# Kernel optimization log

Measured on AMD Instinct MI355X. Metric: run time of the kernel, lower is better.

The kernel has to match this reference:

```python
import jax, jax.numpy as jnp
import numpy as np


def _to_complex(t):
    # last dim 2 = (real, imag) -> complex64
    return jax.lax.complex(t[..., 0], t[..., 1])


def setup_inputs() -> dict:
    key = jax.random.key(0)
    k1, k2, k3, k4 = jax.random.split(key, 4)
    N, C_out, C_in, H, Wf = 2, 64, 3, 256, 129  # Wf = 256//2 + 1 (rfft width)
    X = jax.random.normal(k1, (N, 1, C_in, H, Wf, 2), dtype=jnp.float32)
    D = jax.random.normal(k2, (N, C_out, C_in, H, Wf, 2), dtype=jnp.float32)
    Y = jax.random.normal(k3, (N, C_out, 1, H, Wf, 2), dtype=jnp.float32)
    # alpha is a positive penalty weight; offset away from 0 to avoid blow-up in Z/alpha
    alpha = jax.random.uniform(k4, (N, 1, 1, 1), dtype=jnp.float32) + 0.5
    x_size = np.array([256, 256], dtype=np.int64)  # spatial size for irfft2
    return {"X": X, "D": D, "Y": Y, "alpha": alpha, "x_size": x_size}


def reference(X, D, Y, alpha, x_size):
    C_in = X.shape[2]
    Xc = _to_complex(X)  # (N,1,C_in,H,Wf)
    Dc = _to_complex(D)  # (N,C_out,C_in,H,Wf)
    Yc = _to_complex(Y)  # (N,C_out,1,H,Wf)
    # alpha.unsqueeze(-1).unsqueeze(-1)/C_in: in complex repr one extra axis suffices
    a = (alpha / C_in)[..., None]  # (N,1,1,1,1), real, broadcasts over (N,C_out,C_in,H,Wf)
    Dconj = jnp.conj(Dc)
    Z = Yc * Dc + a * Xc  # (N,C_out,C_in,H,Wf)
    factor1 = Z / a
    numerator = jnp.sum(Dconj * Z, axis=2, keepdims=True)  # (N,C_out,1,H,Wf)
    # csum adds a real scalar (alpha^2) to the real part only
    denominator = a * jnp.sum(Dconj * Dc, axis=2, keepdims=True) + a ** 2
    factor2 = Dc * (numerator / denominator)  # (N,C_out,C_in,H,Wf)
    Xhat = jnp.mean(factor1 - factor2, axis=1)  # (N,C_in,H,Wf)
    Hs, Ws = int(x_size[0]), int(x_size[1])
    # torch.irfft(signal_ndim=2, normalized=False) == full (1/n-normalized) inverse rfft2
    return jnp.fft.irfftn(Xhat, s=(Hs, Ws), axes=(-2, -1))
```

## Files before the change

kernel.cpp:

```cpp
#include <hip/hip_runtime.h>
#include <math.h>

#define H_   256
#define Wf_  129
#define HWf_ 33024
#define CIN_ 3
#define COUT_ 64
#define TW_  0.0245436926f

typedef float f32x4 __attribute__((ext_vector_type(4)));

__global__ __launch_bounds__(256) void solve_stage1(
    const float* __restrict__ X, const float* __restrict__ D,
    const float* __restrict__ Y, const float* __restrict__ alpha,
    float* __restrict__ Xhat)
{
    const int tid  = threadIdx.x;
    const int lane = tid & 63;
    const int cog  = tid >> 6;
    const int pair = blockIdx.x * 64 + lane;
    const int pos0 = pair * 2;
    const int n    = pos0 / HWf_;
    const int hw0  = pos0 - n * HWf_;

    const float a    = alpha[n] * (1.0f / 3.0f);
    const float inva = 1.0f / a;
    const float a2   = a * a;

    f32x4 x[3];
#pragma unroll
    for (int ci = 0; ci < 3; ++ci)
        x[ci] = *(const f32x4*)(X + ((size_t)(n * 3 + ci) * HWf_ + hw0) * 2);

    const int co0 = cog * 16;
    const float* Dp = D + ((size_t)(n * 64 + co0) * 3) * (HWf_ * 2) + hw0 * 2;
    const float* Yp = Y + ((size_t)(n * 64 + co0)) * (HWf_ * 2) + hw0 * 2;

    float acc[12];
#pragma unroll
    for (int q = 0; q < 12; ++q) acc[q] = 0.f;

    for (int cb = 0; cb < 4; ++cb) {
        f32x4 yv[4], dv[12];
#pragma unroll
        for (int j = 0; j < 4; ++j) {
            const int co = cb * 4 + j;
            yv[j]        = __builtin_nontemporal_load(
                               (const f32x4*)(Yp + (size_t)co * (HWf_ * 2)));
            dv[j*3 + 0]  = __builtin_nontemporal_load(
                               (const f32x4*)(Dp + (size_t)(co*3 + 0) * (HWf_ * 2)));
            dv[j*3 + 1]  = __builtin_nontemporal_load(
                               (const f32x4*)(Dp + (size_t)(co*3 + 1) * (HWf_ * 2)));
            dv[j*3 + 2]  = __builtin_nontemporal_load(
                               (const f32x4*)(Dp + (size_t)(co*3 + 2) * (HWf_ * 2)));
        }
#pragma unroll
        for (int j = 0; j < 4; ++j) {
            const f32x4 y  = yv[j];
            const f32x4 d0 = dv[j*3 + 0];
            const f32x4 d1 = dv[j*3 + 1];
            const f32x4 d2 = dv[j*3 + 2];
            {
                float s2 = d0[0]*d0[0] + d0[1]*d0[1] + d1[0]*d1[0] + d1[1]*d1[1]
                         + d2[0]*d2[0] + d2[1]*d2[1];
                float sr = d0[0]*x[0][0] + d0[1]*x[0][1] + d1[0]*x[1][0] + d1[1]*x[1][1]
                         + d2[0]*x[2][0] + d2[1]*x[2][1];
                float si = d0[0]*x[0][1] - d0[1]*x[0][0] + d1[0]*x[1][1] - d1[1]*x[1][0]
                         + d2[0]*x[2][1] - d2[1]*x[2][0];
                float nr = y[0] * s2 + a * sr, ni = y[1] * s2 + a * si;
                float invden = 1.0f / (a * s2 + a2);
                float tr = y[0] * inva - nr * invden;
                float ti = y[1] * inva - ni * invden;
                acc[0] += d0[0]*tr - d0[1]*ti;  acc[1] += d0[0]*ti + d0[1]*tr;
                acc[2] += d1[0]*tr - d1[1]*ti;  acc[3] += d1[0]*ti + d1[1]*tr;
                acc[4] += d2[0]*tr - d2[1]*ti;  acc[5] += d2[0]*ti + d2[1]*tr;
            }
            {
                float s2 = d0[2]*d0[2] + d0[3]*d0[3] + d1[2]*d1[2] + d1[3]*d1[3]
                         + d2[2]*d2[2] + d2[3]*d2[3];
                float sr = d0[2]*x[0][2] + d0[3]*x[0][3] + d1[2]*x[1][2] + d1[3]*x[1][3]
                         + d2[2]*x[2][2] + d2[3]*x[2][3];
                float si = d0[2]*x[0][3] - d0[3]*x[0][2] + d1[2]*x[1][3] - d1[3]*x[1][2]
                         + d2[2]*x[2][3] - d2[3]*x[2][2];
                float nr = y[2] * s2 + a * sr, ni = y[3] * s2 + a * si;
                float invden = 1.0f / (a * s2 + a2);
                float tr = y[2] * inva - nr * invden;
                float ti = y[3] * inva - ni * invden;
                acc[6]  += d0[2]*tr - d0[3]*ti;  acc[7]  += d0[2]*ti + d0[3]*tr;
                acc[8]  += d1[2]*tr - d1[3]*ti;  acc[9]  += d1[2]*ti + d1[3]*tr;
                acc[10] += d2[2]*tr - d2[3]*ti;  acc[11] += d2[2]*ti + d2[3]*tr;
            }
        }
    }

    __shared__ float red[4 * 832];
    {
        const int base = cog * 832 + lane * 13;
#pragma unroll
        for (int q = 0; q < 12; ++q) red[base + q] = acc[q];
    }
    __syncthreads();

#pragma unroll
    for (int it = 0; it < 3; ++it) {
        const int o = tid + 256 * it;
        const int P = o / 12;
        const int r = o - P * 12;
        const int idx = P * 13 + r;
        const float s = red[idx] + red[832 + idx] + red[1664 + idx] + red[2496 + idx];
        const int pos = r / 6;
        const int rr  = r - pos * 6;
        const int ci  = rr >> 1;
        const int cc  = rr & 1;
        const int gp  = (blockIdx.x * 64 + P) * 2 + pos;
        const int hw  = gp - n * HWf_;
        const size_t oa = ((size_t)(n * 3 + ci) * HWf_ + hw) * 2 + cc;
        Xhat[oa] = X[oa] + s * (1.0f / 64.0f);
    }
}

__global__ __launch_bounds__(128) void solve_stage2(
    const float2* __restrict__ in, float2* __restrict__ out)
{
    __shared__ float2 col[256];

    const int b    = blockIdx.x;
    const int n_ci = b / Wf_;
    const int w    = b - n_ci * Wf_;
    const int t    = threadIdx.x;

    const float2* src = in + (size_t)n_ci * HWf_ + w;
    col[t]       = src[t * Wf_];
    col[t + 128] = src[(t + 128) * Wf_];
    __syncthreads();

    float wc, wsn;
    sincosf((float)t * TW_, &wsn, &wc);

    float ar = 0.f, ai = 0.f, br = 0.f, bi = 0.f;
    for (int kb = 0; kb < 8; ++kb) {
        const int k0 = kb * 32;
        float tr, ti;
        {
            const int m = (t * k0) & 255;
            float s, c; sincosf((float)m * TW_, &s, &c);
            tr = c; ti = s;
        }
#pragma unroll
        for (int j = 0; j < 32; ++j) {
            const float2 v = col[k0 + j];
            const float pr = v.x * tr - v.y * ti;
            const float pi = v.x * ti + v.y * tr;
            ar += pr; ai += pi;
            if ((k0 + j) & 1) { br -= pr; bi -= pi; }
            else             { br += pr; bi += pi; }
            const float nt = tr * wc - ti * wsn;
            ti = tr * wsn + ti * wc;
            tr = nt;
        }
    }

    float2* dst = out + (size_t)n_ci * HWf_ + w;
    dst[t * Wf_]         = make_float2(ar * (1.0f / 256.0f), ai * (1.0f / 256.0f));
    dst[(t + 128) * Wf_] = make_float2(br * (1.0f / 256.0f), bi * (1.0f / 256.0f));
}

__global__ __launch_bounds__(128) void solve_stage3(
    const float2* __restrict__ in, float* __restrict__ out)
{
    __shared__ float2 row[Wf_];

    const int b = blockIdx.x;
    const int t = threadIdx.x;

    row[t] = in[(size_t)b * Wf_ + t];
    if (t == 0) row[128] = in[(size_t)b * Wf_ + 128];
    __syncthreads();

    float wc, wsn;
    sincosf((float)t * TW_, &wsn, &wc);

    float sa = 0.f, sb = 0.f;
    for (int kb = 0; kb < 4; ++kb) {
        const int k0 = kb * 32;
        float tr, ti;
        {
            const int m = (t * k0) & 255;
            float s, c; sincosf((float)m * TW_, &s, &c);
            tr = c; ti = s;
        }
#pragma unroll
        for (int j = 0; j < 32; ++j) {
            const float2 v = row[k0 + j];
            const float pr = v.x * tr - v.y * ti;
            sa += pr;
            if ((k0 + j) & 1) sb -= pr; else sb += pr;
            const float nt = tr * wc - ti * wsn;
            ti = tr * wsn + ti * wc;
            tr = nt;
        }
    }

    const float sgn  = (t & 1) ? -1.0f : 1.0f;
    const float base = -0.5f * row[0].x + sgn * 0.5f * row[128].x;
    out[(size_t)b * 256 + t]       = (sa + base) * (1.0f / 128.0f);
    out[(size_t)b * 256 + t + 128] = (sb + base) * (1.0f / 128.0f);
}

extern "C" void kernel_launch(void* const* d_in, const int* in_sizes, int n_in,
                              void* d_out, int out_size, void* d_ws, size_t ws_size,
                              hipStream_t stream) {
    const float* X     = (const float*)d_in[0];
    const float* D     = (const float*)d_in[1];
    const float* Y     = (const float*)d_in[2];
    const float* alpha = (const float*)d_in[3];

    float* ws1 = (float*)d_ws;
    float2* ws2 = (float2*)(ws1 + (size_t)CIN_ * 2 * HWf_ * 2);

    solve_stage1<<<516, 256, 0, stream>>>(X, D, Y, alpha, ws1);
    solve_stage2<<<2 * CIN_ * Wf_, 128, 0, stream>>>((const float2*)ws1, ws2);
    solve_stage3<<<2 * CIN_ * H_, 128, 0, stream>>>(ws2, (float*)d_out);
}
```

Before: 218.6 us.

## Split stage1 output-channel reduction across four blocks with partials summed in stage2

Stage1 now launches four times as many blocks, each covering a quarter of the 64 output channels, with each wave handling four channels instead of sixteen. Each block writes its partial sum to a separate workspace slice. Stage2 adds the four partials plus X while loading its columns. This is meant to raise parallelism and memory-level concurrency in the bandwidth-bound first stage, at the cost of extra partial-sum writes and reads and four times the X loads.

```diff
diff --git a/kernel.cpp b/kernel.cpp
--- a/kernel.cpp
+++ b/kernel.cpp
@@ -7,19 +7,21 @@
 #define CIN_ 3
 #define COUT_ 64
 #define TW_  0.0245436926f
+#define PARTC_ 198144
 
 typedef float f32x4 __attribute__((ext_vector_type(4)));
 
 __global__ __launch_bounds__(256) void solve_stage1(
     const float* __restrict__ X, const float* __restrict__ D,
     const float* __restrict__ Y, const float* __restrict__ alpha,
-    float* __restrict__ Xhat)
+    float* __restrict__ partials)
 {
     const int tid  = threadIdx.x;
     const int lane = tid & 63;
-    const int cog  = tid >> 6;
-    const int pair = blockIdx.x * 64 + lane;
-    const int pos0 = pair * 2;
+    const int wav  = tid >> 6;
+    const int cog  = blockIdx.x & 3;
+    const int pg   = blockIdx.x >> 2;
+    const int pos0 = pg * 128 + lane * 2;
     const int n    = pos0 / HWf_;
     const int hw0  = pos0 - n * HWf_;
 
@@ -32,7 +34,7 @@
     for (int ci = 0; ci < 3; ++ci)
         x[ci] = *(const f32x4*)(X + ((size_t)(n * 3 + ci) * HWf_ + hw0) * 2);
 
-    const int co0 = cog * 16;
+    const int co0 = cog * 16 + wav * 4;
     const float* Dp = D + ((size_t)(n * 64 + co0) * 3) * (HWf_ * 2) + hw0 * 2;
     const float* Yp = Y + ((size_t)(n * 64 + co0)) * (HWf_ * 2) + hw0 * 2;
 
@@ -40,67 +42,66 @@
 #pragma unroll
     for (int q = 0; q < 12; ++q) acc[q] = 0.f;
 
-    for (int cb = 0; cb < 4; ++cb) {
-        f32x4 yv[4], dv[12];
-#pragma unroll
-        for (int j = 0; j < 4; ++j) {
-            const int co = cb * 4 + j;
-            yv[j]        = __builtin_nontemporal_load(
-                               (const f32x4*)(Yp + (size_t)co * (HWf_ * 2)));
-            dv[j*3 + 0]  = __builtin_nontemporal_load(
-                               (const f32x4*)(Dp + (size_t)(co*3 + 0) * (HWf_ * 2)));
-            dv[j*3 + 1]  = __builtin_nontemporal_load(
-                               (const f32x4*)(Dp + (size_t)(co*3 + 1) * (HWf_ * 2)));
-            dv[j*3 + 2]  = __builtin_nontemporal_load(
-                               (const f32x4*)(Dp + (size_t)(co*3 + 2) * (HWf_ * 2)));
-        }
-#pragma unroll
-        for (int j = 0; j < 4; ++j) {
-            const f32x4 y  = yv[j];
-            const f32x4 d0 = dv[j*3 + 0];
-            const f32x4 d1 = dv[j*3 + 1];
-            const f32x4 d2 = dv[j*3 + 2];
-            {
-                float s2 = d0[0]*d0[0] + d0[1]*d0[1] + d1[0]*d1[0] + d1[1]*d1[1]
-                         + d2[0]*d2[0] + d2[1]*d2[1];
-                float sr = d0[0]*x[0][0] + d0[1]*x[0][1] + d1[0]*x[1][0] + d1[1]*x[1][1]
-                         + d2[0]*x[2][0] + d2[1]*x[2][1];
-                float si = d0[0]*x[0][1] - d0[1]*x[0][0] + d1[0]*x[1][1] - d1[1]*x[1][0]
-                         + d2[0]*x[2][1] - d2[1]*x[2][0];
-                float nr = y[0] * s2 + a * sr, ni = y[1] * s2 + a * si;
-                float invden = 1.0f / (a * s2 + a2);
-                float tr = y[0] * inva - nr * invden;
-                float ti = y[1] * inva - ni * invden;
-                acc[0] += d0[0]*tr - d0[1]*ti;  acc[1] += d0[0]*ti + d0[1]*tr;
-                acc[2] += d1[0]*tr - d1[1]*ti;  acc[3] += d1[0]*ti + d1[1]*tr;
-                acc[4] += d2[0]*tr - d2[1]*ti;  acc[5] += d2[0]*ti + d2[1]*tr;
-            }
-            {
-                float s2 = d0[2]*d0[2] + d0[3]*d0[3] + d1[2]*d1[2] + d1[3]*d1[3]
-                         + d2[2]*d2[2] + d2[3]*d2[3];
-                float sr = d0[2]*x[0][2] + d0[3]*x[0][3] + d1[2]*x[1][2] + d1[3]*x[1][3]
-                         + d2[2]*x[2][2] + d2[3]*x[2][3];
-                float si = d0[2]*x[0][3] - d0[3]*x[0][2] + d1[2]*x[1][3] - d1[3]*x[1][2]
-                         + d2[2]*x[2][3] - d2[3]*x[2][2];
-                float nr = y[2] * s2 + a * sr, ni = y[3] * s2 + a * si;
-                float invden = 1.0f / (a * s2 + a2);
-                float tr = y[2] * inva - nr * invden;
-                float ti = y[3] * inva - ni * invden;
-                acc[6]  += d0[2]*tr - d0[3]*ti;  acc[7]  += d0[2]*ti + d0[3]*tr;
-                acc[8]  += d1[2]*tr - d1[3]*ti;  acc[9]  += d1[2]*ti + d1[3]*tr;
-                acc[10] += d2[2]*tr - d2[3]*ti;  acc[11] += d2[2]*ti + d2[3]*tr;
-            }
+    f32x4 yv[4], dv[12];
+#pragma unroll
+    for (int j = 0; j < 4; ++j) {
+        yv[j]       = __builtin_nontemporal_load(
+                          (const f32x4*)(Yp + (size_t)j * (HWf_ * 2)));
+        dv[j*3 + 0] = __builtin_nontemporal_load(
+                          (const f32x4*)(Dp + (size_t)(j*3 + 0) * (HWf_ * 2)));
+        dv[j*3 + 1] = __builtin_nontemporal_load(
+                          (const f32x4*)(Dp + (size_t)(j*3 + 1) * (HWf_ * 2)));
+        dv[j*3 + 2] = __builtin_nontemporal_load(
+                          (const f32x4*)(Dp + (size_t)(j*3 + 2) * (HWf_ * 2)));
+    }
+
+#pragma unroll
+    for (int j = 0; j < 4; ++j) {
+        const f32x4 y  = yv[j];
+        const f32x4 d0 = dv[j*3 + 0];
+        const f32x4 d1 = dv[j*3 + 1];
+        const f32x4 d2 = dv[j*3 + 2];
+        {
+            float s2 = d0[0]*d0[0] + d0[1]*d0[1] + d1[0]*d1[0] + d1[1]*d1[1]
+                     + d2[0]*d2[0] + d2[1]*d2[1];
+            float sr = d0[0]*x[0][0] + d0[1]*x[0][1] + d1[0]*x[1][0] + d1[1]*x[1][1]
+                     + d2[0]*x[2][0] + d2[1]*x[2][1];
+            float si = d0[0]*x[0][1] - d0[1]*x[0][0] + d1[0]*x[1][1] - d1[1]*x[1][0]
+                     + d2[0]*x[2][1] - d2[1]*x[2][0];
+            float nr = y[0] * s2 + a * sr, ni = y[1] * s2 + a * si;
+            float invden = 1.0f / (a * s2 + a2);
+            float tr = y[0] * inva - nr * invden;
+            float ti = y[1] * inva - ni * invden;
+            acc[0] += d0[0]*tr - d0[1]*ti;  acc[1] += d0[0]*ti + d0[1]*tr;
+            acc[2] += d1[0]*tr - d1[1]*ti;  acc[3] += d1[0]*ti + d1[1]*tr;
+            acc[4] += d2[0]*tr - d2[1]*ti;  acc[5] += d2[0]*ti + d2[1]*tr;
+        }
+        {
+            float s2 = d0[2]*d0[2] + d0[3]*d0[3] + d1[2]*d1[2] + d1[3]*d1[3]
+                     + d2[2]*d2[2] + d2[3]*d2[3];
+            float sr = d0[2]*x[0][2] + d0[3]*x[0][3] + d1[2]*x[1][2] + d1[3]*x[1][3]
+                     + d2[2]*x[2][2] + d2[3]*x[2][3];
+            float si = d0[2]*x[0][3] - d0[3]*x[0][2] + d1[2]*x[1][3] - d1[3]*x[1][2]
+                     + d2[2]*x[2][3] - d2[3]*x[2][2];
+            float nr = y[2] * s2 + a * sr, ni = y[3] * s2 + a * si;
+            float invden = 1.0f / (a * s2 + a2);
+            float tr = y[2] * inva - nr * invden;
+            float ti = y[3] * inva - ni * invden;
+            acc[6]  += d0[2]*tr - d0[3]*ti;  acc[7]  += d0[2]*ti + d0[3]*tr;
+            acc[8]  += d1[2]*tr - d1[3]*ti;  acc[9]  += d1[2]*ti + d1[3]*tr;
+            acc[10] += d2[2]*tr - d2[3]*ti;  acc[11] += d2[2]*ti + d2[3]*tr;
         }
     }
 
     __shared__ float red[4 * 832];
     {
-        const int base = cog * 832 + lane * 13;
+        const int base = wav * 832 + lane * 13;
 #pragma unroll
         for (int q = 0; q < 12; ++q) red[base + q] = acc[q];
     }
     __syncthreads();
 
+    float* pb = partials + (size_t)cog * (PARTC_ * 2);
 #pragma unroll
     for (int it = 0; it < 3; ++it) {
         const int o = tid + 256 * it;
@@ -112,15 +113,16 @@
         const int rr  = r - pos * 6;
         const int ci  = rr >> 1;
         const int cc  = rr & 1;
-        const int gp  = (blockIdx.x * 64 + P) * 2 + pos;
+        const int gp  = pg * 128 + P * 2 + pos;
         const int hw  = gp - n * HWf_;
         const size_t oa = ((size_t)(n * 3 + ci) * HWf_ + hw) * 2 + cc;
-        Xhat[oa] = X[oa] + s * (1.0f / 64.0f);
+        pb[oa] = s;
     }
 }
 
 __global__ __launch_bounds__(128) void solve_stage2(
-    const float2* __restrict__ in, float2* __restrict__ out)
+    const float2* __restrict__ Xc, const float2* __restrict__ parts,
+    float2* __restrict__ out)
 {
     __shared__ float2 col[256];
 
@@ -129,9 +131,19 @@
     const int w    = b - n_ci * Wf_;
     const int t    = threadIdx.x;
 
-    const float2* src = in + (size_t)n_ci * HWf_ + w;
-    col[t]       = src[t * Wf_];
-    col[t + 128] = src[(t + 128) * Wf_];
+    const float inv64 = 1.0f / 64.0f;
+#pragma unroll
+    for (int half = 0; half < 2; ++half) {
+        const int h = t + half * 128;
+        const size_t idx = (size_t)n_ci * HWf_ + (size_t)h * Wf_ + w;
+        float2 xv = Xc[idx];
+        float2 p0 = parts[idx];
+        float2 p1 = parts[idx + PARTC_];
+        float2 p2 = parts[idx + 2 * (size_t)PARTC_];
+        float2 p3 = parts[idx + 3 * (size_t)PARTC_];
+        col[h] = make_float2(xv.x + (p0.x + p1.x + p2.x + p3.x) * inv64,
+                             xv.y + (p0.y + p1.y + p2.y + p3.y) * inv64);
+    }
     __syncthreads();
 
     float wc, wsn;
@@ -215,10 +227,11 @@
     const float* Y     = (const float*)d_in[2];
     const float* alpha = (const float*)d_in[3];
 
-    float* ws1 = (float*)d_ws;
-    float2* ws2 = (float2*)(ws1 + (size_t)CIN_ * 2 * HWf_ * 2);
-
-    solve_stage1<<<516, 256, 0, stream>>>(X, D, Y, alpha, ws1);
-    solve_stage2<<<2 * CIN_ * Wf_, 128, 0, stream>>>((const float2*)ws1, ws2);
+    float*  parts = (float*)d_ws;
+    float2* ws2   = (float2*)(parts + 4 * (size_t)PARTC_ * 2);
+
+    solve_stage1<<<2064, 256, 0, stream>>>(X, D, Y, alpha, parts);
+    solve_stage2<<<2 * CIN_ * Wf_, 128, 0, stream>>>(
+        (const float2*)X, (const float2*)parts, ws2);
     solve_stage3<<<2 * CIN_ * H_, 128, 0, stream>>>(ws2, (float*)d_out);
 }
```

Measured after the change: 209.2 us. 1.04x faster.

## Split output-channel reduction across blocks with partial buffers and combine kernel

Applied to the files above, without the earlier changes.

Stage 1 now spreads the 64 output channels over 16 blocks of 4 channels each, writing per-group partial sums to a workspace. A new combine kernel then adds the 16 partials plus X to form Xhat, replacing the in-block shared-memory reduction. This raises the number of blocks and loads in flight for the memory-bound D/Y stream. The cost is extra global traffic for the partials (about 16x the Xhat size), one more kernel launch, and reloading X in every block.

```diff
diff --git a/kernel.cpp b/kernel.cpp
--- a/kernel.cpp
+++ b/kernel.cpp
@@ -4,119 +4,118 @@
 #define H_   256
 #define Wf_  129
 #define HWf_ 33024
+#define NPAIRS_ 16512
 #define CIN_ 3
 #define COUT_ 64
 #define TW_  0.0245436926f
+#define PARTF_ 396288
+#define PART4_ 99072
 
 typedef float f32x4 __attribute__((ext_vector_type(4)));
+#define NTL(p) __builtin_nontemporal_load((const f32x4*)(p))
 
 __global__ __launch_bounds__(256) void solve_stage1(
     const float* __restrict__ X, const float* __restrict__ D,
     const float* __restrict__ Y, const float* __restrict__ alpha,
-    float* __restrict__ Xhat)
-{
-    const int tid  = threadIdx.x;
-    const int lane = tid & 63;
-    const int cog  = tid >> 6;
-    const int pair = blockIdx.x * 64 + lane;
-    const int pos0 = pair * 2;
-    const int n    = pos0 / HWf_;
-    const int hw0  = pos0 - n * HWf_;
+    float* __restrict__ parts)
+{
+    const int tid = threadIdx.x;
+    const int q   = blockIdx.x & 15;
+    const int t2  = blockIdx.x >> 4;
+    const int n   = (t2 >= 33) ? 1 : 0;
+    const int c   = t2 - n * 33;
 
     const float a    = alpha[n] * (1.0f / 3.0f);
     const float inva = 1.0f / a;
     const float a2   = a * a;
 
-    f32x4 x[3];
-#pragma unroll
-    for (int ci = 0; ci < 3; ++ci)
-        x[ci] = *(const f32x4*)(X + ((size_t)(n * 3 + ci) * HWf_ + hw0) * 2);
-
-    const int co0 = cog * 16;
-    const float* Dp = D + ((size_t)(n * 64 + co0) * 3) * (HWf_ * 2) + hw0 * 2;
-    const float* Yp = Y + ((size_t)(n * 64 + co0)) * (HWf_ * 2) + hw0 * 2;
-
-    float acc[12];
-#pragma unroll
-    for (int q = 0; q < 12; ++q) acc[q] = 0.f;
-
-    for (int cb = 0; cb < 4; ++cb) {
-        f32x4 yv[4], dv[12];
-#pragma unroll
-        for (int j = 0; j < 4; ++j) {
-            const int co = cb * 4 + j;
-            yv[j]        = __builtin_nontemporal_load(
-                               (const f32x4*)(Yp + (size_t)co * (HWf_ * 2)));
-            dv[j*3 + 0]  = __builtin_nontemporal_load(
-                               (const f32x4*)(Dp + (size_t)(co*3 + 0) * (HWf_ * 2)));
-            dv[j*3 + 1]  = __builtin_nontemporal_load(
-                               (const f32x4*)(Dp + (size_t)(co*3 + 1) * (HWf_ * 2)));
-            dv[j*3 + 2]  = __builtin_nontemporal_load(
-                               (const f32x4*)(Dp + (size_t)(co*3 + 2) * (HWf_ * 2)));
-        }
-#pragma unroll
-        for (int j = 0; j < 4; ++j) {
-            const f32x4 y  = yv[j];
-            const f32x4 d0 = dv[j*3 + 0];
-            const f32x4 d1 = dv[j*3 + 1];
-            const f32x4 d2 = dv[j*3 + 2];
-            {
-                float s2 = d0[0]*d0[0] + d0[1]*d0[1] + d1[0]*d1[0] + d1[1]*d1[1]
-                         + d2[0]*d2[0] + d2[1]*d2[1];
-                float sr = d0[0]*x[0][0] + d0[1]*x[0][1] + d1[0]*x[1][0] + d1[1]*x[1][1]
-                         + d2[0]*x[2][0] + d2[1]*x[2][1];
-                float si = d0[0]*x[0][1] - d0[1]*x[0][0] + d1[0]*x[1][1] - d1[1]*x[1][0]
-                         + d2[0]*x[2][1] - d2[1]*x[2][0];
-                float nr = y[0] * s2 + a * sr, ni = y[1] * s2 + a * si;
-                float invden = 1.0f / (a * s2 + a2);
-                float tr = y[0] * inva - nr * invden;
-                float ti = y[1] * inva - ni * invden;
-                acc[0] += d0[0]*tr - d0[1]*ti;  acc[1] += d0[0]*ti + d0[1]*tr;
-                acc[2] += d1[0]*tr - d1[1]*ti;  acc[3] += d1[0]*ti + d1[1]*tr;
-                acc[4] += d2[0]*tr - d2[1]*ti;  acc[5] += d2[0]*ti + d2[1]*tr;
+    const int co0 = q * 4;
+    const float* Dbase = D + ((size_t)(n * 64 + co0) * 3) * (HWf_ * 2);
+    const float* Ybase = Y + ((size_t)(n * 64 + co0)) * (HWf_ * 2);
+    const float* Xbase = X + (size_t)n * 3 * (HWf_ * 2);
+    float*       Pq    = parts + (size_t)q * PARTF_ + (size_t)n * 3 * (HWf_ * 2);
+
+#pragma unroll
+    for (int s = 0; s < 2; ++s) {
+        const int pair = c * 512 + s * 256 + tid;
+        if (pair < NPAIRS_) {
+            const int hw0 = pair * 2;
+            const size_t off = (size_t)hw0 * 2;
+
+            f32x4 x0 = *(const f32x4*)(Xbase + 0 * (HWf_ * 2) + off);
+            f32x4 x1 = *(const f32x4*)(Xbase + 1 * (HWf_ * 2) + off);
+            f32x4 x2 = *(const f32x4*)(Xbase + 2 * (HWf_ * 2) + off);
+
+            f32x4 yv[4], dv[12];
+#pragma unroll
+            for (int j = 0; j < 4; ++j) {
+                yv[j]       = NTL(Ybase + (size_t)j * (HWf_ * 2) + off);
+                dv[j*3 + 0] = NTL(Dbase + ((size_t)j * 3 + 0) * (HWf_ * 2) + off);
+                dv[j*3 + 1] = NTL(Dbase + ((size_t)j * 3 + 1) * (HWf_ * 2) + off);
+                dv[j*3 + 2] = NTL(Dbase + ((size_t)j * 3 + 2) * (HWf_ * 2) + off);
             }
-            {
-                float s2 = d0[2]*d0[2] + d0[3]*d0[3] + d1[2]*d1[2] + d1[3]*d1[3]
-                         + d2[2]*d2[2] + d2[3]*d2[3];
-                float sr = d0[2]*x[0][2] + d0[3]*x[0][3] + d1[2]*x[1][2] + d1[3]*x[1][3]
-                         + d2[2]*x[2][2] + d2[3]*x[2][3];
-                float si = d0[2]*x[0][3] - d0[3]*x[0][2] + d1[2]*x[1][3] - d1[3]*x[1][2]
-                         + d2[2]*x[2][3] - d2[3]*x[2][2];
-                float nr = y[2] * s2 + a * sr, ni = y[3] * s2 + a * si;
-                float invden = 1.0f / (a * s2 + a2);
-                float tr = y[2] * inva - nr * invden;
-                float ti = y[3] * inva - ni * invden;
-                acc[6]  += d0[2]*tr - d0[3]*ti;  acc[7]  += d0[2]*ti + d0[3]*tr;
-                acc[8]  += d1[2]*tr - d1[3]*ti;  acc[9]  += d1[2]*ti + d1[3]*tr;
-                acc[10] += d2[2]*tr - d2[3]*ti;  acc[11] += d2[2]*ti + d2[3]*tr;
+
+            float acc[12];
+#pragma unroll
+            for (int k = 0; k < 12; ++k) acc[k] = 0.f;
+
+#pragma unroll
+            for (int j = 0; j < 4; ++j) {
+                const f32x4 y  = yv[j];
+                const f32x4 d0 = dv[j*3 + 0];
+                const f32x4 d1 = dv[j*3 + 1];
+                const f32x4 d2 = dv[j*3 + 2];
+                {
+                    float s2 = d0[0]*d0[0] + d0[1]*d0[1] + d1[0]*d1[0] + d1[1]*d1[1]
+                             + d2[0]*d2[0] + d2[1]*d2[1];
+                    float sr = d0[0]*x0[0] + d0[1]*x0[1] + d1[0]*x1[0] + d1[1]*x1[1]
+                             + d2[0]*x2[0] + d2[1]*x2[1];
+                    float si = d0[0]*x0[1] - d0[1]*x0[0] + d1[0]*x1[1] - d1[1]*x1[0]
+                             + d2[0]*x2[1] - d2[1]*x2[0];
+                    float nr = y[0] * s2 + a * sr, ni = y[1] * s2 + a * si;
+                    float invden = 1.0f / (a * s2 + a2);
+                    float tr = y[0] * inva - nr * invden;
+                    float ti = y[1] * inva - ni * invden;
+                    acc[0] += d0[0]*tr - d0[1]*ti;  acc[1] += d0[0]*ti + d0[1]*tr;
+                    acc[4] += d1[0]*tr - d1[1]*ti;  acc[5] += d1[0]*ti + d1[1]*tr;
+                    acc[8] += d2[0]*tr - d2[1]*ti;  acc[9] += d2[0]*ti + d2[1]*tr;
+                }
+                {
+                    float s2 = d0[2]*d0[2] + d0[3]*d0[3] + d1[2]*d1[2] + d1[3]*d1[3]
+                             + d2[2]*d2[2] + d2[3]*d2[3];
+                    float sr = d0[2]*x0[2] + d0[3]*x0[3] + d1[2]*x1[2] + d1[3]*x1[3]
+                             + d2[2]*x2[2] + d2[3]*x2[3];
+                    float si = d0[2]*x0[3] - d0[3]*x0[2] + d1[2]*x1[3] - d1[3]*x1[2]
+                             + d2[2]*x2[3] - d2[3]*x2[2];
+                    float nr = y[2] * s2 + a * sr, ni = y[3] * s2 + a * si;
+                    float invden = 1.0f / (a * s2 + a2);
+                    float tr = y[2] * inva - nr * invden;
+                    float ti = y[3] * inva - ni * invden;
+                    acc[2]  += d0[2]*tr - d0[3]*ti;  acc[3]  += d0[2]*ti + d0[3]*tr;
+                    acc[6]  += d1[2]*tr - d1[3]*ti;  acc[7]  += d1[2]*ti + d1[3]*tr;
+                    acc[10] += d2[2]*tr - d2[3]*ti;  acc[11] += d2[2]*ti + d2[3]*tr;
+                }
             }
+
+#pragma unroll
+            for (int ci = 0; ci < 3; ++ci) {
+                f32x4 v; v[0] = acc[ci*4+0]; v[1] = acc[ci*4+1];
+                         v[2] = acc[ci*4+2]; v[3] = acc[ci*4+3];
+                *(f32x4*)(Pq + (size_t)ci * (HWf_ * 2) + off) = v;
+            }
         }
     }
-
-    __shared__ float red[4 * 832];
-    {
-        const int base = cog * 832 + lane * 13;
-#pragma unroll
-        for (int q = 0; q < 12; ++q) red[base + q] = acc[q];
-    }
-    __syncthreads();
-
-#pragma unroll
-    for (int it = 0; it < 3; ++it) {
-        const int o = tid + 256 * it;
-        const int P = o / 12;
-        const int r = o - P * 12;
-        const int idx = P * 13 + r;
-        const float s = red[idx] + red[832 + idx] + red[1664 + idx] + red[2496 + idx];
-        const int pos = r / 6;
-        const int rr  = r - pos * 6;
-        const int ci  = rr >> 1;
-        const int cc  = rr & 1;
-        const int gp  = (blockIdx.x * 64 + P) * 2 + pos;
-        const int hw  = gp - n * HWf_;
-        const size_t oa = ((size_t)(n * 3 + ci) * HWf_ + hw) * 2 + cc;
-        Xhat[oa] = X[oa] + s * (1.0f / 64.0f);
-    }
+}
+
+__global__ __launch_bounds__(256) void solve_combine(
+    const f32x4* __restrict__ X4, const f32x4* __restrict__ P4,
+    f32x4* __restrict__ out4)
+{
+    const int i = blockIdx.x * 256 + threadIdx.x;
+    f32x4 s = P4[i];
+#pragma unroll
+    for (int k = 1; k < 16; ++k) s += P4[i + (size_t)k * PART4_];
+    out4[i] = X4[i] + s * (1.0f / 64.0f);
 }
 
 __global__ __launch_bounds__(128) void solve_stage2(
@@ -143,8 +142,8 @@
         float tr, ti;
         {
             const int m = (t * k0) & 255;
-            float s, c; sincosf((float)m * TW_, &s, &c);
-            tr = c; ti = s;
+            float s, c2; sincosf((float)m * TW_, &s, &c2);
+            tr = c2; ti = s;
         }
 #pragma unroll
         for (int j = 0; j < 32; ++j) {
@@ -186,8 +185,8 @@
         float tr, ti;
         {
             const int m = (t * k0) & 255;
-            float s, c; sincosf((float)m * TW_, &s, &c);
-            tr = c; ti = s;
+            float s, c2; sincosf((float)m * TW_, &s, &c2);
+            tr = c2; ti = s;
         }
 #pragma unroll
         for (int j = 0; j < 32; ++j) {
@@ -215,10 +214,13 @@
     const float* Y     = (const float*)d_in[2];
     const float* alpha = (const float*)d_in[3];
 
-    float* ws1 = (float*)d_ws;
-    float2* ws2 = (float2*)(ws1 + (size_t)CIN_ * 2 * HWf_ * 2);
-
-    solve_stage1<<<516, 256, 0, stream>>>(X, D, Y, alpha, ws1);
-    solve_stage2<<<2 * CIN_ * Wf_, 128, 0, stream>>>((const float2*)ws1, ws2);
+    float*  parts = (float*)d_ws;
+    float*  xhat  = parts + (size_t)16 * PARTF_;
+    float2* ws2   = (float2*)(xhat + PARTF_);
+
+    solve_stage1<<<1056, 256, 0, stream>>>(X, D, Y, alpha, parts);
+    solve_combine<<<387, 256, 0, stream>>>(
+        (const f32x4*)X, (const f32x4*)parts, (f32x4*)xhat);
+    solve_stage2<<<2 * CIN_ * Wf_, 128, 0, stream>>>((const float2*)xhat, ws2);
     solve_stage3<<<2 * CIN_ * H_, 128, 0, stream>>>(ws2, (float*)d_out);
 }
```

Measured after the change: 209.8 us. -4.0%, faster.
